# Kernel optimization log

Measured on AMD Instinct MI355X. Metric: run time of the kernel, lower is better.

## Reference

```python
import jax, jax.numpy as jnp
import numpy as np

N_NODES = 100000
N_EDGES = 1000000
VOCAB = 128
EMB = 64
HID = 64
N_CLASSES = 2
N_GRAPHS = 2048


def setup_inputs() -> dict:
    key = jax.random.key(0)
    ks = jax.random.split(key, 12)
    x = jax.random.randint(ks[0], (N_NODES,), 0, VOCAB)
    edge_index = jax.random.randint(ks[1], (2, N_EDGES), 0, N_NODES)
    batch = jnp.sort(jax.random.randint(ks[2], (N_NODES,), 0, N_GRAPHS))

    def glorot(k, shape):
        fan = shape[0]
        return jax.random.normal(k, shape, dtype=jnp.float32) / np.sqrt(fan).astype(np.float32)

    emb = jax.random.normal(ks[3], (VOCAB, EMB), dtype=jnp.float32)
    W1_l = glorot(ks[4], (EMB, HID)); b1 = jnp.zeros((HID,), jnp.float32)
    W1_r = glorot(ks[5], (EMB, HID))
    W2_l = glorot(ks[6], (HID, HID)); b2 = jnp.zeros((HID,), jnp.float32)
    W2_r = glorot(ks[7], (HID, HID))
    W_out = glorot(ks[8], (HID, N_CLASSES)); b_out = jnp.zeros((N_CLASSES,), jnp.float32)
    return {"x": x, "edge_index": edge_index, "batch": batch, "emb": emb,
            "W1_l": W1_l, "b1": b1, "W1_r": W1_r,
            "W2_l": W2_l, "b2": b2, "W2_r": W2_r,
            "W_out": W_out, "b_out": b_out}


def _sage_conv(h, src, dst, Wl, bl, Wr):
    # PyG SAGEConv: out = lin_l(mean_{j in N(i)} h_j) + lin_r(h_i); lin_r has no bias
    msgs = h[src]                                                        # [E, D] gather
    agg = jax.ops.segment_sum(msgs, dst, num_segments=N_NODES)          # [N, D] scatter-add
    cnt = jax.ops.segment_sum(jnp.ones((src.shape[0], 1), h.dtype), dst,
                              num_segments=N_NODES)                      # [N, 1] degree
    mean = agg / jnp.maximum(cnt, 1.0)
    return mean @ Wl + bl + h @ Wr


def reference(x, edge_index, batch, emb, W1_l, b1, W1_r, W2_l, b2, W2_r, W_out, b_out):
    src, dst = edge_index[0], edge_index[1]
    h = emb[x]                                                           # [N, EMB]
    h = jax.nn.relu(_sage_conv(h, src, dst, W1_l, b1, W1_r))             # [N, HID]
    h = jax.nn.relu(_sage_conv(h, src, dst, W2_l, b2, W2_r))             # [N, HID]
    # global_mean_pool over graph ids
    gsum = jax.ops.segment_sum(h, batch, num_segments=N_GRAPHS)          # [G, HID]
    gcnt = jax.ops.segment_sum(jnp.ones((N_NODES, 1), h.dtype), batch,
                               num_segments=N_GRAPHS)
    pooled = gsum / jnp.maximum(gcnt, 1.0)
    return pooled @ W_out + b_out                                        # [G, C]
```

## Files before the change

kernel.cpp:

```cpp
#include <hip/hip_runtime.h>
#include <hip/hip_bf16.h>

#define N_NODES 100000
#define N_EDGES 1000000
#define EMB 64
#define HID 64
#define VOCAB 128
#define N_GRAPHS 2048

#define CBUCKET 256
#define NBK ((N_NODES + CBUCKET - 1) / CBUCKET)
#define CAP 4096
#define CHUNK 4096
#define SCAT_BLOCKS ((N_EDGES + CHUNK - 1) / CHUNK)
#define GB ((N_NODES + 255) / 256)

#define BCASTF(v, l) __int_as_float(__builtin_amdgcn_readlane(__float_as_int(v), (l)))

typedef __attribute__((ext_vector_type(8))) short short8;
typedef __attribute__((ext_vector_type(4))) float f32x4;
typedef __attribute__((ext_vector_type(2))) float f32x2;

__device__ __forceinline__ float bf2f(unsigned short u) {
    return __uint_as_float((unsigned)u << 16);
}
__device__ __forceinline__ unsigned short f2bf(float f) {
    return __bfloat16_as_ushort(__float2bfloat16(f));
}

__global__ __launch_bounds__(256) void scatter_kernel(
    const int* __restrict__ src, const int* __restrict__ dst,
    const int* __restrict__ x,
    int* __restrict__ cursor, unsigned* __restrict__ edge8,
    const int* __restrict__ batch, int* __restrict__ gstart,
    const float* __restrict__ emb, const float* __restrict__ W1l,
    const float* __restrict__ W1r,
    const float* __restrict__ W2l, const float* __restrict__ W2r,
    float* __restrict__ embW1l, float* __restrict__ embW1r,
    unsigned short* __restrict__ w2frag, unsigned char* __restrict__ p8z)
{
    __shared__ unsigned earr[CHUNK];
    __shared__ unsigned short karr[CHUNK];
    __shared__ int bcnt[NBK];
    __shared__ int bbase[NBK];
    int b = blockIdx.x;
    int t = threadIdx.x;

    if (b < SCAT_BLOCKS) {
        for (int i = t; i < NBK; i += 256) bcnt[i] = 0;
        __syncthreads();
        int e0 = b * CHUNK;
        int n = min(e0 + CHUNK, N_EDGES) - e0;
        for (int i = t; i < n; i += 256) {
            int d = dst[e0 + i];
            int s = src[e0 + i];
            int xv = x[s];
            int k = d >> 8;
            earr[i] = (unsigned)s | ((unsigned)xv << 17) | ((unsigned)(d & 255) << 24);
            karr[i] = (unsigned short)k;
            atomicAdd(&bcnt[k], 1);
        }
        __syncthreads();
        for (int i = t; i < NBK; i += 256) {
            int c = bcnt[i];
            bbase[i] = i * CAP + (c ? atomicAdd(&cursor[i], c) : 0);
            bcnt[i] = 0;
        }
        __syncthreads();
        for (int i = t; i < n; i += 256) {
            int k = karr[i];
            int off = atomicAdd(&bcnt[k], 1);
            edge8[bbase[k] + off] = earr[i];
        }
    } else if (b < SCAT_BLOCKS + GB) {
        int i = (b - SCAT_BLOCKS) * 256 + t;
        if (i >= N_NODES) return;
        int bg = batch[i];
        int bp = (i == 0) ? -1 : batch[i - 1];
        for (int g = bp + 1; g <= bg; ++g) gstart[g] = i;
        if (i == N_NODES - 1)
            for (int g = bg + 1; g <= N_GRAPHS; ++g) gstart[g] = N_NODES;
    } else {
        int vb = b - SCAT_BLOCKS - GB;
        if (vb == 0 && t < 16)
            ((unsigned*)(p8z + (size_t)N_NODES * 64))[t] = 0u;
        int wave = t >> 6, lane = t & 63;
        int v = vb * 4 + wave;
        if (v < VOCAB) {
            float er = emb[v * 64 + lane];
            float al = 0.f, ar = 0.f;
#pragma unroll 8
            for (int d = 0; d < 64; ++d) {
                float e = BCASTF(er, d);
                al += e * W1l[d * 64 + lane];
                ar += e * W1r[d * 64 + lane];
            }
            embW1l[v * 64 + lane] = al;
            embW1r[v * 64 + lane] = ar;
        }
        int g = vb * 256 + t;
        int j = g & 7, l = (g >> 3) & 63, h = (g >> 9) & 1, tt = g >> 10;
        int k = h * 32 + ((l >> 4) * 8) + j;
        int n = tt * 16 + (l & 15);
        float w = (n < 64) ? W2l[k * 64 + n] : W2r[k * 64 + (n - 64)];
        w2frag[g] = f2bf(w);
    }
}

__global__ __launch_bounds__(256) void csr_kernel(
    const unsigned* __restrict__ edge8, const int* __restrict__ cursor,
    int* __restrict__ row_start, int* __restrict__ deg, int* __restrict__ col)
{
    __shared__ int cnt[CBUCKET];
    __shared__ int scn[CBUCKET];
    int b = blockIdx.x;
    int t = threadIdx.x;
    int lo = b * CAP, hi = lo + cursor[b];
    cnt[t] = 0;
    __syncthreads();
    for (int i = lo + t; i < hi; i += 256)
        atomicAdd(&cnt[edge8[i] >> 24], 1);
    __syncthreads();
    int v = cnt[t];
    scn[t] = v;
    __syncthreads();
    for (int off = 1; off < 256; off <<= 1) {
        int tmp = (t >= off) ? scn[t - off] : 0;
        __syncthreads();
        scn[t] += tmp;
        __syncthreads();
    }
    int excl = scn[t] - v;
    int node = b * CBUCKET + t;
    if (node < N_NODES) { row_start[node] = lo + excl; deg[node] = v; }
    cnt[t] = excl;
    __syncthreads();
    for (int i = lo + t; i < hi; i += 256) {
        unsigned e = edge8[i];
        int slot = atomicAdd(&cnt[e >> 24], 1);
        col[lo + slot] = (int)(e & 0xFFFFFF);
    }
}

#define S1_NPW 8
__global__ __launch_bounds__(256) void sage1_kernel(
    const int* __restrict__ x, const float* __restrict__ embW1l,
    const float* __restrict__ embW1r, const float* __restrict__ b1,
    const int* __restrict__ row_start, const int* __restrict__ deg,
    const int* __restrict__ col, const unsigned short* __restrict__ w2frag,
    unsigned char* __restrict__ p8, unsigned short* __restrict__ q16)
{
    __shared__ float elds[VOCAB * 64];
    int t = threadIdx.x;
    for (int i = t * 4; i < VOCAB * 64; i += 1024)
        *(float4*)&elds[i] = *(const float4*)&embW1l[i];
    __syncthreads();

    int wave = t >> 6, lane = t & 63;
    int block_base = blockIdx.x * (4 * S1_NPW);
    int base_node = block_base + wave * S1_NPW;
    int c = lane & 15;
    int g = lane >> 4;
    float4 bias4 = ((const float4*)b1)[c];

    int rs[S1_NPW], dgs[S1_NPW], cidx[S1_NPW], xn[S1_NPW];
    float4 self4[S1_NPW];
#pragma unroll
    for (int n = 0; n < S1_NPW; ++n) {
        rs[n] = row_start[base_node + n];
        dgs[n] = deg[base_node + n];
        xn[n] = x[base_node + n];
    }
#pragma unroll
    for (int n = 0; n < S1_NPW; ++n) {
        cidx[n] = (lane < dgs[n]) ? col[rs[n] + lane] : 0;
        self4[n] = ((const float4*)(embW1r + xn[n] * 64))[c];
    }

    unsigned short* msbuf = (unsigned short*)elds;
    ushort4 h1row[S1_NPW];

    for (int n = 0; n < S1_NPW; ++n) {
        int dg = dgs[n];
        int dgc = (dg < 64) ? dg : 64;

        float4 a0 = {0.f,0.f,0.f,0.f}, a1 = {0.f,0.f,0.f,0.f};
        for (int j = 0; j < dgc; j += 8) {
            int jj0 = j + g, jj1 = j + 4 + g;
            int x0 = __shfl(cidx[n], jj0, 64) >> 17;
            int x1 = __shfl(cidx[n], jj1, 64) >> 17;
            float4 v0 = *(const float4*)&elds[x0 * 64 + c * 4];
            float4 v1 = *(const float4*)&elds[x1 * 64 + c * 4];
            if (jj0 < dgc) { a0.x += v0.x; a0.y += v0.y; a0.z += v0.z; a0.w += v0.w; }
            if (jj1 < dgc) { a1.x += v1.x; a1.y += v1.y; a1.z += v1.z; a1.w += v1.w; }
        }
        for (int k = 64; k < dg; ++k) {
            int cc = col[rs[n] + k] >> 17;
            float4 v = *(const float4*)&elds[cc * 64 + c * 4];
            if (g == 0) { a0.x += v.x; a0.y += v.y; a0.z += v.z; a0.w += v.w; }
        }
        float sx = a0.x + a1.x, sy = a0.y + a1.y, sz = a0.z + a1.z, sw = a0.w + a1.w;
        sx += __shfl_xor(sx, 16, 64); sx += __shfl_xor(sx, 32, 64);
        sy += __shfl_xor(sy, 16, 64); sy += __shfl_xor(sy, 32, 64);
        sz += __shfl_xor(sz, 16, 64); sz += __shfl_xor(sz, 32, 64);
        sw += __shfl_xor(sw, 16, 64); sw += __shfl_xor(sw, 32, 64);

        float inv = 1.0f / fmaxf((float)dg, 1.0f);
        h1row[n].x = f2bf(fmaxf(sx * inv + bias4.x + self4[n].x, 0.f));
        h1row[n].y = f2bf(fmaxf(sy * inv + bias4.y + self4[n].y, 0.f));
        h1row[n].z = f2bf(fmaxf(sz * inv + bias4.z + self4[n].z, 0.f));
        h1row[n].w = f2bf(fmaxf(sw * inv + bias4.w + self4[n].w, 0.f));
    }
    __syncthreads();

    if (g == 0) {
#pragma unroll
        for (int n = 0; n < S1_NPW; ++n)
            *(ushort4*)&msbuf[(wave * S1_NPW + n) * 72 + c * 4] = h1row[n];
    }
    __syncthreads();

    int grp = wave >> 1, tbase = (wave & 1) * 4;
    int m = lane & 15, quad = lane >> 4;
    int base16g = block_base + grp * 16;
    const unsigned short* arow = &msbuf[(grp * 16 + m) * 72 + quad * 8];
    short8 a0 = *(const short8*)(arow);
    short8 a1 = *(const short8*)(arow + 32);

#pragma unroll
    for (int tt = tbase; tt < tbase + 4; ++tt) {
        short8 b0 = *(const short8*)(w2frag + tt * 1024 + lane * 8);
        short8 b1v = *(const short8*)(w2frag + tt * 1024 + 512 + lane * 8);
        f32x4 acc = {0.f, 0.f, 0.f, 0.f};
        acc = __builtin_amdgcn_mfma_f32_16x16x32_bf16(a0, b0, acc, 0, 0, 0);
        acc = __builtin_amdgcn_mfma_f32_16x16x32_bf16(a1, b1v, acc, 0, 0, 0);
        int o = tt * 16 + m;
        if (o < 64) {
            int pk01 = __builtin_amdgcn_cvt_pk_fp8_f32(acc[0], acc[1], 0, false);
            int pk23 = __builtin_amdgcn_cvt_pk_fp8_f32(acc[2], acc[3], 0, false);
            p8[(base16g + quad * 4 + 0) * 64 + o] = (unsigned char)(pk01 & 0xff);
            p8[(base16g + quad * 4 + 1) * 64 + o] = (unsigned char)((pk01 >> 8) & 0xff);
            p8[(base16g + quad * 4 + 2) * 64 + o] = (unsigned char)(pk23 & 0xff);
            p8[(base16g + quad * 4 + 3) * 64 + o] = (unsigned char)((pk23 >> 8) & 0xff);
        } else {
            int oc = o & 63;
#pragma unroll
            for (int i = 0; i < 4; ++i)
                q16[(base16g + quad * 4 + i) * 64 + oc] = f2bf(acc[i]);
        }
    }
}

#define S2_NPW 8
#define ZROW N_NODES
__global__ __launch_bounds__(256, 6) void sage2_kernel(
    const unsigned char* __restrict__ p, const unsigned short* __restrict__ q,
    const int* __restrict__ row_start, const int* __restrict__ deg,
    const int* __restrict__ col, const float* __restrict__ b2,
    const float* __restrict__ Wout, const int* __restrict__ batch,
    float* __restrict__ gsum)
{
    int t = threadIdx.x;
    int wave = t >> 6, lane = t & 63;
    int base_node = (blockIdx.x * 4 + wave) * S2_NPW;
    int c = lane & 15;
    int g = lane >> 4;

    float4 b2v = ((const float4*)b2)[c];
    float4 w01 = ((const float4*)Wout)[c * 2];
    float4 w23 = ((const float4*)Wout)[c * 2 + 1];

    int rs[S2_NPW], dgs[S2_NPW], cidx[S2_NPW];
#pragma unroll
    for (int n = 0; n < S2_NPW; ++n) {
        rs[n] = row_start[base_node + n];
        dgs[n] = deg[base_node + n];
    }
#pragma unroll
    for (int n = 0; n < S2_NPW; ++n)
        cidx[n] = (lane < dgs[n]) ? (col[rs[n] + lane] & 0x1FFFF) : ZROW;

#define ACC(a, v) { f32x2 f01_ = __builtin_amdgcn_cvt_pk_f32_fp8((int)(v), false); \
                    f32x2 f23_ = __builtin_amdgcn_cvt_pk_f32_fp8((int)(v), true);  \
                    (a).x += f01_.x; (a).y += f01_.y; (a).z += f23_.x; (a).w += f23_.y; }

#pragma unroll
    for (int n = 0; n < S2_NPW; n += 2) {
        int dgA = dgs[n], dgB = dgs[n + 1];

        int iA0 = __shfl(cidx[n], g, 64);
        int iA1 = __shfl(cidx[n], 4 + g, 64);
        int iA2 = __shfl(cidx[n], 8 + g, 64);
        int iA3 = __shfl(cidx[n], 12 + g, 64);
        int iB0 = __shfl(cidx[n + 1], g, 64);
        int iB1 = __shfl(cidx[n + 1], 4 + g, 64);
        int iB2 = __shfl(cidx[n + 1], 8 + g, 64);
        int iB3 = __shfl(cidx[n + 1], 12 + g, 64);

        unsigned vA0 = *(const unsigned*)(p + (size_t)iA0 * 64 + c * 4);
        unsigned vA1 = *(const unsigned*)(p + (size_t)iA1 * 64 + c * 4);
        unsigned vA2 = *(const unsigned*)(p + (size_t)iA2 * 64 + c * 4);
        unsigned vA3 = *(const unsigned*)(p + (size_t)iA3 * 64 + c * 4);
        unsigned vB0 = *(const unsigned*)(p + (size_t)iB0 * 64 + c * 4);
        unsigned vB1 = *(const unsigned*)(p + (size_t)iB1 * 64 + c * 4);
        unsigned vB2 = *(const unsigned*)(p + (size_t)iB2 * 64 + c * 4);
        unsigned vB3 = *(const unsigned*)(p + (size_t)iB3 * 64 + c * 4);

        float4 aA = {0.f,0.f,0.f,0.f}, aB = {0.f,0.f,0.f,0.f};
        ACC(aA, vA0) ACC(aA, vA1) ACC(aA, vA2) ACC(aA, vA3)
        ACC(aB, vB0) ACC(aB, vB1) ACC(aB, vB2) ACC(aB, vB3)

        for (int j = 16; j < dgA; j += 8) {
            int i0 = __shfl(cidx[n], j + g, 64);
            int i1 = __shfl(cidx[n], j + 4 + g, 64);
            unsigned v0 = *(const unsigned*)(p + (size_t)i0 * 64 + c * 4);
            unsigned v1 = *(const unsigned*)(p + (size_t)i1 * 64 + c * 4);
            ACC(aA, v0) ACC(aA, v1)
        }
        for (int j = 16; j < dgB; j += 8) {
            int i0 = __shfl(cidx[n + 1], j + g, 64);
            int i1 = __shfl(cidx[n + 1], j + 4 + g, 64);
            unsigned v0 = *(const unsigned*)(p + (size_t)i0 * 64 + c * 4);
            unsigned v1 = *(const unsigned*)(p + (size_t)i1 * 64 + c * 4);
            ACC(aB, v0) ACC(aB, v1)
        }
        for (int k = 64; k < dgA; ++k) {
            int r = col[rs[n] + k] & 0x1FFFF;
            unsigned v = *(const unsigned*)(p + (size_t)r * 64 + c * 4);
            if (g == 0) ACC(aA, v)
        }
        for (int k = 64; k < dgB; ++k) {
            int r = col[rs[n + 1] + k] & 0x1FFFF;
            unsigned v = *(const unsigned*)(p + (size_t)r * 64 + c * 4);
            if (g == 0) ACC(aB, v)
        }

        aA.x += __shfl_xor(aA.x, 16, 64); aA.y += __shfl_xor(aA.y, 16, 64);
        aA.z += __shfl_xor(aA.z, 16, 64); aA.w += __shfl_xor(aA.w, 16, 64);
        aB.x += __shfl_xor(aB.x, 16, 64); aB.y += __shfl_xor(aB.y, 16, 64);
        aB.z += __shfl_xor(aB.z, 16, 64); aB.w += __shfl_xor(aB.w, 16, 64);
        aA.x += __shfl_xor(aA.x, 32, 64); aA.y += __shfl_xor(aA.y, 32, 64);
        aA.z += __shfl_xor(aA.z, 32, 64); aA.w += __shfl_xor(aA.w, 32, 64);
        aB.x += __shfl_xor(aB.x, 32, 64); aB.y += __shfl_xor(aB.y, 32, 64);
        aB.z += __shfl_xor(aB.z, 32, 64); aB.w += __shfl_xor(aB.w, 32, 64);

#pragma unroll
        for (int e = 0; e < 2; ++e) {
            int node = base_node + n + e;
            int dg = (e == 0) ? dgA : dgB;
            float4 a = (e == 0) ? aA : aB;
            float inv = 1.0f / fmaxf((float)dg, 1.0f);
            ushort4 qv = *(const ushort4*)(q + node * 64 + c * 4);
            float h0 = fmaxf(a.x * inv + b2v.x + bf2f(qv.x), 0.f);
            float h1 = fmaxf(a.y * inv + b2v.y + bf2f(qv.y), 0.f);
            float h2 = fmaxf(a.z * inv + b2v.z + bf2f(qv.z), 0.f);
            float h3 = fmaxf(a.w * inv + b2v.w + bf2f(qv.w), 0.f);

            float p0 = h0 * w01.x + h1 * w01.z + h2 * w23.x + h3 * w23.z;
            float p1 = h0 * w01.y + h1 * w01.w + h2 * w23.y + h3 * w23.w;
            if (g != 0) { p0 = 0.f; p1 = 0.f; }
            p0 += __shfl_down(p0, 8, 64);  p1 += __shfl_down(p1, 8, 64);
            p0 += __shfl_down(p0, 4, 64);  p1 += __shfl_down(p1, 4, 64);
            p0 += __shfl_down(p0, 2, 64);  p1 += __shfl_down(p1, 2, 64);
            p0 += __shfl_down(p0, 1, 64);  p1 += __shfl_down(p1, 1, 64);
            if (lane == 0) {
                int grp = batch[node];
                atomicAdd(&gsum[grp * 2 + 0], p0);
                atomicAdd(&gsum[grp * 2 + 1], p1);
            }
        }
    }
#undef ACC
}

__global__ __launch_bounds__(256) void finalize_kernel(
    const float* __restrict__ gsum, const int* __restrict__ gstart,
    const float* __restrict__ bout, float* __restrict__ out)
{
    int g = blockIdx.x * 256 + threadIdx.x;
    if (g >= N_GRAPHS) return;
    int cnt = gstart[g + 1] - gstart[g];
    float inv = 1.0f / fmaxf((float)cnt, 1.0f);
    out[g * 2 + 0] = gsum[g * 2 + 0] * inv + bout[0];
    out[g * 2 + 1] = gsum[g * 2 + 1] * inv + bout[1];
}

extern "C" void kernel_launch(void* const* d_in, const int* in_sizes, int n_in,
                              void* d_out, int out_size, void* d_ws, size_t ws_size,
                              hipStream_t stream) {
    const int*   x    = (const int*)  d_in[0];
    const int*   ei   = (const int*)  d_in[1];
    const int*   batch= (const int*)  d_in[2];
    const float* emb  = (const float*)d_in[3];
    const float* W1l  = (const float*)d_in[4];
    const float* b1   = (const float*)d_in[5];
    const float* W1r  = (const float*)d_in[6];
    const float* W2l  = (const float*)d_in[7];
    const float* b2   = (const float*)d_in[8];
    const float* W2r  = (const float*)d_in[9];
    const float* Wout = (const float*)d_in[10];
    const float* bout = (const float*)d_in[11];
    float* out = (float*)d_out;

    const int* src = ei;
    const int* dst = ei + N_EDGES;

    char* ws = (char*)d_ws;
    size_t off = 0;
    unsigned char*  p8     = (unsigned char*) (ws + off); off += (size_t)N_NODES * 64 + 64;
    unsigned short* q16    = (unsigned short*)(ws + off); off += (size_t)N_NODES * 64 * 2;
    unsigned short* w2frag = (unsigned short*)(ws + off); off += (size_t)8192 * 2;
    float*    embW1l = (float*)   (ws + off); off += (size_t)VOCAB * 64 * 4;
    float*    embW1r = (float*)   (ws + off); off += (size_t)VOCAB * 64 * 4;
    int*      rowst  = (int*)     (ws + off); off += (size_t)N_NODES * 4;
    int*      deg    = (int*)     (ws + off); off += (size_t)N_NODES * 4;
    int*      col    = (int*)     (ws + off); off += (size_t)(NBK * CAP + 256) * 4;
    unsigned* edge8  = (unsigned*)(ws + off); off += (size_t)NBK * CAP * 4;
    int*      gstart = (int*)     (ws + off); off += (size_t)(N_GRAPHS + 1) * 4;
    int*      cursor = (int*)     (ws + off); off += (size_t)NBK * 4;
    float*    gsum   = (float*)   (ws + off); off += (size_t)N_GRAPHS * 2 * 4;

    hipMemsetAsync(cursor, 0, (size_t)NBK * 4 + (size_t)N_GRAPHS * 2 * 4, stream);

    scatter_kernel<<<SCAT_BLOCKS + GB + 32, 256, 0, stream>>>(
        src, dst, x, cursor, edge8,
        batch, gstart, emb, W1l, W1r, W2l, W2r, embW1l, embW1r, w2frag, p8);
    csr_kernel<<<NBK, 256, 0, stream>>>(edge8, cursor, rowst, deg, col);
    sage1_kernel<<<N_NODES / (4 * S1_NPW), 256, 0, stream>>>(
        x, embW1l, embW1r, b1, rowst, deg, col, w2frag, p8, q16);
    sage2_kernel<<<N_NODES / (4 * S2_NPW), 256, 0, stream>>>(
        p8, q16, rowst, deg, col, b2, Wout, batch, gsum);
    finalize_kernel<<<(N_GRAPHS + 255) / 256, 256, 0, stream>>>(gsum, gstart, bout, out);
}
```

Baseline: 209.2 us.

## Compute layer-1 aggregation as vocab histogram times embedding weights via MFMA

```diff
diff --git a/kernel.cpp b/kernel.cpp
--- a/kernel.cpp
+++ b/kernel.cpp
@@ -109,12 +109,30 @@
 
 __global__ __launch_bounds__(256) void csr_kernel(
     const unsigned* __restrict__ edge8, const int* __restrict__ cursor,
-    int* __restrict__ row_start, int* __restrict__ deg, int* __restrict__ col)
+    int* __restrict__ row_start, int* __restrict__ deg, int* __restrict__ col,
+    const float* __restrict__ embW1l, const float* __restrict__ embW1r,
+    unsigned short* __restrict__ w1frag)
 {
     __shared__ int cnt[CBUCKET];
     __shared__ int scn[CBUCKET];
     int b = blockIdx.x;
     int t = threadIdx.x;
+
+    if (b < 8) {
+        int g0 = (b * 256 + t) * 8;
+#pragma unroll
+        for (int j = 0; j < 8; ++j) {
+            int g = g0 + j;
+            int fi = g >> 9;
+            int kf = fi >> 2, nt = fi & 3;
+            int l = (g >> 3) & 63, jj = g & 7;
+            int kg = kf * 32 + ((l >> 4) << 3) + jj;
+            int n = nt * 16 + (l & 15);
+            float w = (kg < 128) ? embW1l[kg * 64 + n] : embW1r[(kg - 128) * 64 + n];
+            w1frag[g] = f2bf(w);
+        }
+    }
+
     int lo = b * CAP, hi = lo + cursor[b];
     cnt[t] = 0;
     __syncthreads();
@@ -142,111 +160,137 @@
     }
 }
 
-#define S1_NPW 8
 __global__ __launch_bounds__(256) void sage1_kernel(
-    const int* __restrict__ x, const float* __restrict__ embW1l,
-    const float* __restrict__ embW1r, const float* __restrict__ b1,
-    const int* __restrict__ row_start, const int* __restrict__ deg,
-    const int* __restrict__ col, const unsigned short* __restrict__ w2frag,
+    const int* __restrict__ x, const int* __restrict__ deg,
+    const unsigned* __restrict__ edge8, const int* __restrict__ cursor,
+    const unsigned short* __restrict__ w1frag,
+    const unsigned short* __restrict__ w2frag, const float* __restrict__ b1,
     unsigned char* __restrict__ p8, unsigned short* __restrict__ q16)
 {
-    __shared__ float elds[VOCAB * 64];
+    __shared__ unsigned hist[128 * 32];
+    __shared__ unsigned short msbuf[128 * 72];
+    __shared__ int xl[128];
+    __shared__ float invd[128];
+
+    int blk = blockIdx.x, bucket = blk >> 1, half = blk & 1;
     int t = threadIdx.x;
-    for (int i = t * 4; i < VOCAB * 64; i += 1024)
-        *(float4*)&elds[i] = *(const float4*)&embW1l[i];
+    int nbase = bucket * CBUCKET + half * 128;
+
+    for (int i = t * 4; i < 128 * 32; i += 1024)
+        *(uint4*)&hist[i] = (uint4){0u, 0u, 0u, 0u};
+    if (t < 128) {
+        int node = nbase + t;
+        int dv = (node < N_NODES) ? deg[node] : 0;
+        invd[t] = 1.0f / fmaxf((float)dv, 1.0f);
+        xl[t] = (node < N_NODES) ? x[node] : 0;
+    }
+    __syncthreads();
+
+    int lo = bucket * CAP, ecnt = cursor[bucket];
+    for (int i = t; i < ecnt; i += 256) {
+        unsigned e = edge8[lo + i];
+        int ld = (int)(e >> 24);
+        if ((ld >> 7) == half) {
+            int r = ld & 127;
+            int xv = (int)((e >> 17) & 127);
+            int wc = (xv >> 2) ^ ((r & 7) << 2);
+            atomicAdd(&hist[r * 32 + wc], 1u << ((xv & 3) * 8));
+        }
+    }
     __syncthreads();
 
     int wave = t >> 6, lane = t & 63;
-    int block_base = blockIdx.x * (4 * S1_NPW);
-    int base_node = block_base + wave * S1_NPW;
-    int c = lane & 15;
-    int g = lane >> 4;
-    float4 bias4 = ((const float4*)b1)[c];
-
-    int rs[S1_NPW], dgs[S1_NPW], cidx[S1_NPW], xn[S1_NPW];
-    float4 self4[S1_NPW];
-#pragma unroll
-    for (int n = 0; n < S1_NPW; ++n) {
-        rs[n] = row_start[base_node + n];
-        dgs[n] = deg[base_node + n];
-        xn[n] = x[base_node + n];
-    }
-#pragma unroll
-    for (int n = 0; n < S1_NPW; ++n) {
-        cidx[n] = (lane < dgs[n]) ? col[rs[n] + lane] : 0;
-        self4[n] = ((const float4*)(embW1r + xn[n] * 64))[c];
-    }
-
-    unsigned short* msbuf = (unsigned short*)elds;
-    ushort4 h1row[S1_NPW];
-
-    for (int n = 0; n < S1_NPW; ++n) {
-        int dg = dgs[n];
-        int dgc = (dg < 64) ? dg : 64;
-
-        float4 a0 = {0.f,0.f,0.f,0.f}, a1 = {0.f,0.f,0.f,0.f};
-        for (int j = 0; j < dgc; j += 8) {
-            int jj0 = j + g, jj1 = j + 4 + g;
-            int x0 = __shfl(cidx[n], jj0, 64) >> 17;
-            int x1 = __shfl(cidx[n], jj1, 64) >> 17;
-            float4 v0 = *(const float4*)&elds[x0 * 64 + c * 4];
-            float4 v1 = *(const float4*)&elds[x1 * 64 + c * 4];
-            if (jj0 < dgc) { a0.x += v0.x; a0.y += v0.y; a0.z += v0.z; a0.w += v0.w; }
-            if (jj1 < dgc) { a1.x += v1.x; a1.y += v1.y; a1.z += v1.z; a1.w += v1.w; }
-        }
-        for (int k = 64; k < dg; ++k) {
-            int cc = col[rs[n] + k] >> 17;
-            float4 v = *(const float4*)&elds[cc * 64 + c * 4];
-            if (g == 0) { a0.x += v.x; a0.y += v.y; a0.z += v.z; a0.w += v.w; }
-        }
-        float sx = a0.x + a1.x, sy = a0.y + a1.y, sz = a0.z + a1.z, sw = a0.w + a1.w;
-        sx += __shfl_xor(sx, 16, 64); sx += __shfl_xor(sx, 32, 64);
-        sy += __shfl_xor(sy, 16, 64); sy += __shfl_xor(sy, 32, 64);
-        sz += __shfl_xor(sz, 16, 64); sz += __shfl_xor(sz, 32, 64);
-        sw += __shfl_xor(sw, 16, 64); sw += __shfl_xor(sw, 32, 64);
-
-        float inv = 1.0f / fmaxf((float)dg, 1.0f);
-        h1row[n].x = f2bf(fmaxf(sx * inv + bias4.x + self4[n].x, 0.f));
-        h1row[n].y = f2bf(fmaxf(sy * inv + bias4.y + self4[n].y, 0.f));
-        h1row[n].z = f2bf(fmaxf(sz * inv + bias4.z + self4[n].z, 0.f));
-        h1row[n].w = f2bf(fmaxf(sw * inv + bias4.w + self4[n].w, 0.f));
-    }
-    __syncthreads();
-
-    if (g == 0) {
-#pragma unroll
-        for (int n = 0; n < S1_NPW; ++n)
-            *(ushort4*)&msbuf[(wave * S1_NPW + n) * 72 + c * 4] = h1row[n];
-    }
-    __syncthreads();
-
-    int grp = wave >> 1, tbase = (wave & 1) * 4;
-    int m = lane & 15, quad = lane >> 4;
-    int base16g = block_base + grp * 16;
-    const unsigned short* arow = &msbuf[(grp * 16 + m) * 72 + quad * 8];
-    short8 a0 = *(const short8*)(arow);
-    short8 a1 = *(const short8*)(arow + 32);
-
-#pragma unroll
-    for (int tt = tbase; tt < tbase + 4; ++tt) {
-        short8 b0 = *(const short8*)(w2frag + tt * 1024 + lane * 8);
-        short8 b1v = *(const short8*)(w2frag + tt * 1024 + 512 + lane * 8);
-        f32x4 acc = {0.f, 0.f, 0.f, 0.f};
-        acc = __builtin_amdgcn_mfma_f32_16x16x32_bf16(a0, b0, acc, 0, 0, 0);
-        acc = __builtin_amdgcn_mfma_f32_16x16x32_bf16(a1, b1v, acc, 0, 0, 0);
-        int o = tt * 16 + m;
-        if (o < 64) {
-            int pk01 = __builtin_amdgcn_cvt_pk_fp8_f32(acc[0], acc[1], 0, false);
-            int pk23 = __builtin_amdgcn_cvt_pk_fp8_f32(acc[2], acc[3], 0, false);
-            p8[(base16g + quad * 4 + 0) * 64 + o] = (unsigned char)(pk01 & 0xff);
-            p8[(base16g + quad * 4 + 1) * 64 + o] = (unsigned char)((pk01 >> 8) & 0xff);
-            p8[(base16g + quad * 4 + 2) * 64 + o] = (unsigned char)(pk23 & 0xff);
-            p8[(base16g + quad * 4 + 3) * 64 + o] = (unsigned char)((pk23 >> 8) & 0xff);
-        } else {
-            int oc = o & 63;
-#pragma unroll
-            for (int i = 0; i < 4; ++i)
-                q16[(base16g + quad * 4 + i) * 64 + oc] = f2bf(acc[i]);
+    int m = lane & 15;
+    int qd = lane >> 4;
+    int hswz = (m & 7) << 2;
+
+#pragma unroll
+    for (int rt = wave * 2; rt < wave * 2 + 2; ++rt) {
+        short8 acnt[4], aself[4];
+#pragma unroll
+        for (int kf = 0; kf < 4; ++kf) {
+            int w0 = (kf * 8 + qd * 2) ^ hswz;
+            uint2 u = *(const uint2*)&hist[(rt * 16 + m) * 32 + w0];
+            short8 f;
+            f[0] = (short)f2bf((float)(u.x & 255));
+            f[1] = (short)f2bf((float)((u.x >> 8) & 255));
+            f[2] = (short)f2bf((float)((u.x >> 16) & 255));
+            f[3] = (short)f2bf((float)(u.x >> 24));
+            f[4] = (short)f2bf((float)(u.y & 255));
+            f[5] = (short)f2bf((float)((u.y >> 8) & 255));
+            f[6] = (short)f2bf((float)((u.y >> 16) & 255));
+            f[7] = (short)f2bf((float)(u.y >> 24));
+            acnt[kf] = f;
+        }
+        int xv = xl[rt * 16 + m];
+#pragma unroll
+        for (int kf = 0; kf < 4; ++kf) {
+            int v = xv - kf * 32 - qd * 8;
+            short8 f;
+#pragma unroll
+            for (int j = 0; j < 8; ++j)
+                f[j] = (v == j) ? (short)0x3F80 : (short)0;
+            aself[kf] = f;
+        }
+        float iv0 = invd[rt * 16 + qd * 4 + 0];
+        float iv1 = invd[rt * 16 + qd * 4 + 1];
+        float iv2 = invd[rt * 16 + qd * 4 + 2];
+        float iv3 = invd[rt * 16 + qd * 4 + 3];
+
+#pragma unroll
+        for (int nt = 0; nt < 4; ++nt) {
+            f32x4 accA = {0.f, 0.f, 0.f, 0.f};
+            f32x4 accS = {0.f, 0.f, 0.f, 0.f};
+#pragma unroll
+            for (int kf = 0; kf < 4; ++kf) {
+                short8 bA = *(const short8*)(w1frag + ((kf * 4 + nt) * 64 + lane) * 8);
+                accA = __builtin_amdgcn_mfma_f32_16x16x32_bf16(acnt[kf], bA, accA, 0, 0, 0);
+            }
+#pragma unroll
+            for (int kf = 0; kf < 4; ++kf) {
+                short8 bS = *(const short8*)(w1frag + (((kf + 4) * 4 + nt) * 64 + lane) * 8);
+                accS = __builtin_amdgcn_mfma_f32_16x16x32_bf16(aself[kf], bS, accS, 0, 0, 0);
+            }
+            int c = nt * 16 + m;
+            float b1c = b1[c];
+            int rb = rt * 16 + qd * 4;
+            msbuf[(rb + 0) * 72 + c] = f2bf(fmaxf(accA[0] * iv0 + accS[0] + b1c, 0.f));
+            msbuf[(rb + 1) * 72 + c] = f2bf(fmaxf(accA[1] * iv1 + accS[1] + b1c, 0.f));
+            msbuf[(rb + 2) * 72 + c] = f2bf(fmaxf(accA[2] * iv2 + accS[2] + b1c, 0.f));
+            msbuf[(rb + 3) * 72 + c] = f2bf(fmaxf(accA[3] * iv3 + accS[3] + b1c, 0.f));
+        }
+    }
+    __syncthreads();
+
+#pragma unroll
+    for (int rt = wave * 2; rt < wave * 2 + 2; ++rt) {
+        const unsigned short* arow = &msbuf[(rt * 16 + m) * 72 + qd * 8];
+        short8 a0 = *(const short8*)(arow);
+        short8 a1 = *(const short8*)(arow + 32);
+        int rowb = nbase + rt * 16 + qd * 4;
+
+#pragma unroll
+        for (int tt = 0; tt < 8; ++tt) {
+            short8 b0 = *(const short8*)(w2frag + tt * 1024 + lane * 8);
+            short8 b1v = *(const short8*)(w2frag + tt * 1024 + 512 + lane * 8);
+            f32x4 acc = {0.f, 0.f, 0.f, 0.f};
+            acc = __builtin_amdgcn_mfma_f32_16x16x32_bf16(a0, b0, acc, 0, 0, 0);
+            acc = __builtin_amdgcn_mfma_f32_16x16x32_bf16(a1, b1v, acc, 0, 0, 0);
+            int o = tt * 16 + m;
+            if (o < 64) {
+                int pk01 = __builtin_amdgcn_cvt_pk_fp8_f32(acc[0], acc[1], 0, false);
+                int pk23 = __builtin_amdgcn_cvt_pk_fp8_f32(acc[2], acc[3], 0, false);
+                if (rowb + 0 < N_NODES) p8[(rowb + 0) * 64 + o] = (unsigned char)(pk01 & 0xff);
+                if (rowb + 1 < N_NODES) p8[(rowb + 1) * 64 + o] = (unsigned char)((pk01 >> 8) & 0xff);
+                if (rowb + 2 < N_NODES) p8[(rowb + 2) * 64 + o] = (unsigned char)(pk23 & 0xff);
+                if (rowb + 3 < N_NODES) p8[(rowb + 3) * 64 + o] = (unsigned char)((pk23 >> 8) & 0xff);
+            } else {
+                int oc = o & 63;
+#pragma unroll
+                for (int i = 0; i < 4; ++i)
+                    if (rowb + i < N_NODES)
+                        q16[(rowb + i) * 64 + oc] = f2bf(acc[i]);
+            }
         }
     }
 }
@@ -410,6 +454,7 @@
     unsigned char*  p8     = (unsigned char*) (ws + off); off += (size_t)N_NODES * 64 + 64;
     unsigned short* q16    = (unsigned short*)(ws + off); off += (size_t)N_NODES * 64 * 2;
     unsigned short* w2frag = (unsigned short*)(ws + off); off += (size_t)8192 * 2;
+    unsigned short* w1frag = (unsigned short*)(ws + off); off += (size_t)16384 * 2;
     float*    embW1l = (float*)   (ws + off); off += (size_t)VOCAB * 64 * 4;
     float*    embW1r = (float*)   (ws + off); off += (size_t)VOCAB * 64 * 4;
     int*      rowst  = (int*)     (ws + off); off += (size_t)N_NODES * 4;
@@ -425,9 +470,10 @@
     scatter_kernel<<<SCAT_BLOCKS + GB + 32, 256, 0, stream>>>(
         src, dst, x, cursor, edge8,
         batch, gstart, emb, W1l, W1r, W2l, W2r, embW1l, embW1r, w2frag, p8);
-    csr_kernel<<<NBK, 256, 0, stream>>>(edge8, cursor, rowst, deg, col);
-    sage1_kernel<<<N_NODES / (4 * S1_NPW), 256, 0, stream>>>(
-        x, embW1l, embW1r, b1, rowst, deg, col, w2frag, p8, q16);
+    csr_kernel<<<NBK, 256, 0, stream>>>(edge8, cursor, rowst, deg, col,
+                                        embW1l, embW1r, w1frag);
+    sage1_kernel<<<NBK * 2, 256, 0, stream>>>(
+        x, deg, edge8, cursor, w1frag, w2frag, b1, p8, q16);
     sage2_kernel<<<N_NODES / (4 * S2_NPW), 256, 0, stream>>>(
         p8, q16, rowst, deg, col, b2, Wout, batch, gsum);
     finalize_kernel<<<(N_GRAPHS + 255) / 256, 256, 0, stream>>>(gsum, gstart, bout, out);
```

After: 190.9 us. 1.1x faster.
